# Kernel tuning notes

Hardware: AMD Instinct MI355X
Metric: run time of the kernel (lower is better)

## Reference

```python
import jax, jax.numpy as jnp
import numpy as np

VOL = 100.0  # cubic volume (100,100,100)


def _forward(x, positions, input_weights, features, output_weights,
             connection_radii, thresholds, n_iterations):
    # clamp positions into the volume (per-axis, min 0.1, max VOL-0.1)
    pos = jnp.clip(positions, 0.1, VOL - 0.1)                      # [N,3]
    radii = jnp.clip(connection_radii, 1.0, 50.0)                  # [N]
    # pairwise Euclidean distances via ||a||^2 + ||b||^2 - 2ab (avoids [N,N,3])
    sq = jnp.sum(pos * pos, axis=1)
    d2 = jnp.maximum(sq[:, None] + sq[None, :] - 2.0 * (pos @ pos.T), 0.0)
    pos_mask = d2 > 0.0
    dist = jnp.where(pos_mask, jnp.sqrt(jnp.where(pos_mask, d2, 1.0)), 0.0)  # [N,N]
    max_r = jnp.max(radii)
    conn_mask = (dist < max_r).astype(dist.dtype)
    atten = jnp.exp(-jnp.minimum(dist / (radii[:, None] + 1e-6), 20.0)) * conn_mask
    # feature similarity (F.normalize uses eps as a clamp-min on the norm)
    fn = features / jnp.maximum(jnp.linalg.norm(features, axis=1, keepdims=True), 1e-6)
    feat_sim = fn @ fn.T                                            # [N,N]
    cw = atten * (0.3 + 0.7 * jnp.clip(feat_sim, -1.0, 1.0))
    cw = cw / (jnp.sum(cw, axis=1, keepdims=True) + 1e-6)           # row-normalized [N,N]
    # spatial input / output gating along x-axis
    xc = jnp.clip(pos[:, 0] / VOL, 0.0, 1.0)                        # [N]
    iw = jnp.exp(-3.0 * xc)
    iw = iw / (jnp.sum(iw) + 1e-6)
    act = (x @ input_weights.T) * iw                                # [B,N]
    for _ in range(n_iterations):
        act = jnp.minimum(jax.nn.relu(act + act @ cw.T - thresholds), 100.0)
    ow = jnp.exp(3.0 * (xc - 1.0))
    ow = ow / (jnp.sum(ow) + 1e-6)
    return (act * ow) @ output_weights                              # [B,out]


def setup_inputs() -> dict:
    key = jax.random.key(0)
    ks = jax.random.split(key, 5)
    N, IN, OUT, FD, B = 8000, 784, 10, 32, 64
    return {
        "x": jax.random.normal(ks[0], (B, IN), jnp.float32),
        "positions": jax.random.uniform(ks[1], (N, 3), jnp.float32) * VOL,
        "input_weights": jax.random.normal(ks[2], (N, IN), jnp.float32) * 0.01,
        "features": jax.random.normal(ks[3], (N, FD), jnp.float32) * 0.1,
        "output_weights": jax.random.normal(ks[4], (N, OUT), jnp.float32) * 0.01,
        "connection_radii": jnp.ones((N,), jnp.float32) * 15.0,
        "thresholds": jnp.zeros((N,), jnp.float32),
        "n_iterations": 2,
    }


def reference(x, positions, input_weights, features, output_weights,
              connection_radii, thresholds, n_iterations):
    return _forward(x, positions, input_weights, features, output_weights,
                    connection_radii, thresholds, n_iterations)
```

## Files before the change

kernel.cpp:

```cpp
#include <hip/hip_runtime.h>
#include <hip/hip_bf16.h>
#include <math.h>

#define VOLF 100.0f
#define FD 32
#define OUT_DIM 10
#define MAXN 320
#define MAX_LAUNCH_ITERS 4
#define OB 128
#define CHUNK 28
#define NCHUNK 7
#define LDP 68
#define PS 8
#define NCD 5
#define CELLW 20.0f
#define NCELL (NCD*NCD)

__global__ __launch_bounds__(256) void k_prext(
    const float* __restrict__ x, const float* __restrict__ positions,
    const float* __restrict__ radii_in, const float* __restrict__ features,
    float* __restrict__ xT, float* __restrict__ posx4,
    float* __restrict__ radii, float* __restrict__ e_iw, float* __restrict__ e_ow,
    float* __restrict__ fn, float* __restrict__ scal, int N, int IN, int nxt)
{
    __shared__ float tile[64][65];
    __shared__ float red[256];
    if ((int)blockIdx.x < nxt) {
        int w = threadIdx.x >> 6, lane = threadIdx.x & 63;
        int k0 = blockIdx.x * 64;
        #pragma unroll
        for (int r = 0; r < 16; r++) {
            int b = w * 16 + r;
            int k = k0 + lane;
            if (k < IN) tile[lane][b] = x[(size_t)b * IN + k];
        }
        __syncthreads();
        #pragma unroll
        for (int r = 0; r < 16; r++) {
            int kl = w * 16 + r;
            int k = k0 + kl;
            if (k < IN) xT[(size_t)k * 64 + lane] = tile[kl][lane];
        }
        return;
    }
    int i = (blockIdx.x - nxt) * 256 + threadIdx.x;
    float my_iw = 0.0f, my_ow = 0.0f, my_r = 0.0f;
    if (i < N) {
        float px = fminf(fmaxf(positions[3*i+0], 0.1f), VOLF - 0.1f);
        float py = fminf(fmaxf(positions[3*i+1], 0.1f), VOLF - 0.1f);
        float pz = fminf(fmaxf(positions[3*i+2], 0.1f), VOLF - 0.1f);
        float sq = px*px + py*py + pz*pz;
        posx4[4*i+0] = px; posx4[4*i+1] = py; posx4[4*i+2] = pz; posx4[4*i+3] = sq;
        float r = fminf(fmaxf(radii_in[i], 1.0f), 50.0f);
        radii[i] = r; my_r = r;
        float xc = fminf(fmaxf(px / VOLF, 0.0f), 1.0f);
        my_iw = expf(-3.0f * xc);
        my_ow = expf(3.0f * (xc - 1.0f));
        e_iw[i] = my_iw; e_ow[i] = my_ow;
        float s = 0.0f;
        #pragma unroll
        for (int k = 0; k < FD; k++) { float v = features[(size_t)i*FD + k]; s += v*v; }
        float nrm = fmaxf(sqrtf(s), 1e-6f);
        #pragma unroll
        for (int k = 0; k < FD; k++) fn[(size_t)i*FD + k] = features[(size_t)i*FD + k] / nrm;
    }
    red[threadIdx.x] = my_iw; __syncthreads();
    for (int s = 128; s > 0; s >>= 1) { if (threadIdx.x < s) red[threadIdx.x] += red[threadIdx.x + s]; __syncthreads(); }
    if (threadIdx.x == 0) atomicAdd(&scal[0], red[0]);
    __syncthreads();
    red[threadIdx.x] = my_ow; __syncthreads();
    for (int s = 128; s > 0; s >>= 1) { if (threadIdx.x < s) red[threadIdx.x] += red[threadIdx.x + s]; __syncthreads(); }
    if (threadIdx.x == 0) atomicAdd(&scal[1], red[0]);
    if (i < N) atomicMax((int*)&scal[2], __float_as_int(my_r));
}

__global__ __launch_bounds__(64) void k_binfill(
    const float* __restrict__ posx4, float4* __restrict__ posb, int* __restrict__ jmap,
    int* __restrict__ binoff, int* __restrict__ bincnt, int N)
{
    int c = blockIdx.x, lane = threadIdx.x;
    int offs = 0, mine = 0;
    for (int jb = 0; jb < N; jb += 64) {
        float4 q = ((const float4*)posx4)[jb + lane];
        int ix = min(NCD-1, (int)(q.x * (1.0f/CELLW)));
        int iy = min(NCD-1, (int)(q.y * (1.0f/CELLW)));
        int cj = ix * NCD + iy;
        offs += (int)__popcll(__ballot(cj < c));
        mine += (int)__popcll(__ballot(cj == c));
    }
    unsigned long long lmask = (1ull << lane) - 1ull;
    int w = 0;
    for (int jb = 0; jb < N; jb += 64) {
        int j = jb + lane;
        float4 q = ((const float4*)posx4)[j];
        int ix = min(NCD-1, (int)(q.x * (1.0f/CELLW)));
        int iy = min(NCD-1, (int)(q.y * (1.0f/CELLW)));
        bool hit = (ix * NCD + iy == c);
        unsigned long long m = __ballot(hit);
        if (hit) {
            int pos = offs + w + (int)__popcll(m & lmask);
            posb[pos] = q;
            jmap[pos] = j;
        }
        w += (int)__popcll(m);
    }
    if (lane == 0) { binoff[c] = offs; bincnt[c] = mine; }
}

__global__ __launch_bounds__(256) void k_act0(
    const float* __restrict__ xT, const float* __restrict__ Wi,
    float* __restrict__ partial, int N, int IN)
{
    __shared__ float smem[2 * 64 * 68];
    float* wtT = smem;
    int t = threadIdx.x;
    int wave = t >> 6, lane = t & 63;
    int nr = lane >> 2, br = lane & 3;
    int i0 = blockIdx.x * 64;
    int kbase = blockIdx.y * 196;
    float acc[4][16];
    #pragma unroll
    for (int a = 0; a < 4; a++)
        #pragma unroll
        for (int b = 0; b < 16; b++) acc[a][b] = 0.0f;

    for (int c = 0; c < NCHUNK; c++) {
        int k0 = kbase + c * CHUNK;
        __syncthreads();
        for (int fi = t; fi < 64 * (CHUNK/4); fi += 256) {
            int n = fi / (CHUNK/4), q = fi % (CHUNK/4);
            float4 w4 = *(const float4*)(Wi + (size_t)(i0 + n) * IN + k0 + q * 4);
            wtT[(q*4+0)*LDP + n] = w4.x;
            wtT[(q*4+1)*LDP + n] = w4.y;
            wtT[(q*4+2)*LDP + n] = w4.z;
            wtT[(q*4+3)*LDP + n] = w4.w;
        }
        __syncthreads();
        for (int q = ((wave + c) & 3); q < CHUNK/4; q += 4) {
            #pragma unroll
            for (int j = 0; j < 4; j++) {
                int kl = q*4 + j;
                float4 a4 = *(const float4*)(&wtT[kl * LDP + nr*4]);
                const float* xr = xT + (size_t)(k0 + kl) * 64 + br*16;
                float4 b0 = *(const float4*)(xr + 0);
                float4 b1 = *(const float4*)(xr + 4);
                float4 b2 = *(const float4*)(xr + 8);
                float4 b3 = *(const float4*)(xr + 12);
                #pragma unroll
                for (int a = 0; a < 4; a++) {
                    float av = (a==0) ? a4.x : (a==1) ? a4.y : (a==2) ? a4.z : a4.w;
                    acc[a][ 0] += av*b0.x; acc[a][ 1] += av*b0.y; acc[a][ 2] += av*b0.z; acc[a][ 3] += av*b0.w;
                    acc[a][ 4] += av*b1.x; acc[a][ 5] += av*b1.y; acc[a][ 6] += av*b1.z; acc[a][ 7] += av*b1.w;
                    acc[a][ 8] += av*b2.x; acc[a][ 9] += av*b2.y; acc[a][10] += av*b2.z; acc[a][11] += av*b2.w;
                    acc[a][12] += av*b3.x; acc[a][13] += av*b3.y; acc[a][14] += av*b3.z; acc[a][15] += av*b3.w;
                }
            }
        }
    }
    __syncthreads();
    float4* sm4 = (float4*)smem;
    int g = wave >> 1;
    if (wave & 1) {
        #pragma unroll
        for (int a = 0; a < 4; a++)
            #pragma unroll
            for (int b4 = 0; b4 < 4; b4++)
                sm4[(g*16 + a*4 + b4) * 64 + lane] =
                    make_float4(acc[a][b4*4+0], acc[a][b4*4+1], acc[a][b4*4+2], acc[a][b4*4+3]);
    }
    __syncthreads();
    if (!(wave & 1)) {
        int slot = blockIdx.y * 2 + g;
        size_t pbase = ((size_t)slot * N + i0 + nr*4) * 64 + br*16;
        #pragma unroll
        for (int a = 0; a < 4; a++)
            #pragma unroll
            for (int b4 = 0; b4 < 4; b4++) {
                float4 o = sm4[(g*16 + a*4 + b4) * 64 + lane];
                o.x += acc[a][b4*4+0]; o.y += acc[a][b4*4+1];
                o.z += acc[a][b4*4+2]; o.w += acc[a][b4*4+3];
                *(float4*)(partial + pbase + (size_t)a * 64 + b4*4) = o;
            }
    }
}

__global__ __launch_bounds__(256) void k_act0_red(
    const float* __restrict__ partial, const float* __restrict__ e_iw,
    const float* __restrict__ scal, float* __restrict__ actA, int N)
{
    int idx = blockIdx.x * 256 + threadIdx.x;
    int i = idx >> 6;
    size_t stride = (size_t)N * 64;
    float s = 0.0f;
    #pragma unroll
    for (int p = 0; p < PS; p++) s += partial[p * stride + idx];
    float inv = 1.0f / (scal[0] + 1e-6f);
    actA[idx] = s * (e_iw[i] * inv);
}

__device__ __forceinline__ void scan_body(
    const float4& p, const float4& q, int j, float maxr, bool act,
    unsigned long long lmask, int2* __restrict__ ep, size_t base, int& cnt)
{
    float d2 = fmaxf(p.w + q.w - 2.0f*(p.x*q.x + p.y*q.y + p.z*q.z), 0.0f);
    float dist = sqrtf(d2);
    bool hit = act && (dist < maxr);
    unsigned long long m = __ballot(hit);
    if (m) {
        if (hit) {
            int pos = cnt + (int)__popcll(m & lmask);
            if (pos < MAXN) ep[base + pos] = make_int2(j, __float_as_int(dist));
        }
        cnt += (int)__popcll(m);
    }
}

__global__ __launch_bounds__(256) void k_scan(
    const float4* __restrict__ posb, const int* __restrict__ jmap,
    const float* __restrict__ scal, int2* __restrict__ ep, int* __restrict__ nbr_cnt,
    const int* __restrict__ binoff, const int* __restrict__ bincnt, int N)
{
    int wave = threadIdx.x >> 6, lane = threadIdx.x & 63;
    int s0 = (blockIdx.x * 4 + wave) * 2;
    float4 p0 = posb[s0], p1 = posb[s0 + 1];
    int r0 = jmap[s0], r1 = jmap[s0 + 1];
    float maxr = __int_as_float(((const int*)scal)[2]);
    int R = (int)ceilf(maxr * (1.0f/CELLW));
    int cxa = min(NCD-1, (int)(p0.x * (1.0f/CELLW))), cya = min(NCD-1, (int)(p0.y * (1.0f/CELLW)));
    int cxb = min(NCD-1, (int)(p1.x * (1.0f/CELLW))), cyb = min(NCD-1, (int)(p1.y * (1.0f/CELLW)));
    int ix0 = max(0, min(cxa, cxb) - R), ix1 = min(NCD-1, max(cxa, cxb) + R);
    int iy0 = max(0, min(cya, cyb) - R), iy1 = min(NCD-1, max(cya, cyb) + R);
    unsigned long long lmask = (1ull << lane) - 1ull;
    int c0 = 0, c1 = 0;
    size_t base0 = (size_t)r0 * MAXN, base1 = (size_t)r1 * MAXN;
    for (int ix = ix0; ix <= ix1; ix++)
    for (int iy = iy0; iy <= iy1; iy++) {
        int c = ix * NCD + iy;
        int bs = binoff[c], cnt = bincnt[c];
        for (int sb = 0; sb < cnt; sb += 64) {
            bool act = (sb + lane) < cnt;
            int s = act ? (bs + sb + lane) : bs;
            float4 q = posb[s];
            int j = jmap[s];
            scan_body(p0, q, j, maxr, act, lmask, ep, base0, c0);
            scan_body(p1, q, j, maxr, act, lmask, ep, base1, c1);
        }
    }
    if (lane == 0) {
        nbr_cnt[r0] = min(c0, MAXN);
        nbr_cnt[r1] = min(c1, MAXN);
    }
}

__global__ __launch_bounds__(256) void k_weight(
    const float* __restrict__ fn, const float* __restrict__ radii,
    int2* __restrict__ ep ,
    const int* __restrict__ nbr_cnt, float* __restrict__ rowinv, int N)
{
    int i = blockIdx.x;
    int lane = threadIdx.x & 63;
    int wave = threadIdx.x >> 6;
    int sub = lane & 7;
    int eg  = lane >> 3;
    float4 fni = ((const float4*)(fn + (size_t)i * FD))[sub];
    float inv_ri = 1.0f / (radii[i] + 1e-6f);
    int cnt = nbr_cnt[i];
    float s = 0.0f;
    for (int e0 = wave * 8; e0 < cnt; e0 += 32) {
        int e = e0 + eg;
        bool act = e < cnt;
        int ecl = act ? e : (cnt - 1);
        int2 edge = ep[(size_t)i * MAXN + ecl];
        int j      = edge.x;
        float dist = __int_as_float(edge.y);
        float4 fj = ((const float4*)(fn + (size_t)j * FD))[sub];
        float fs = fni.x*fj.x + fni.y*fj.y + fni.z*fj.z + fni.w*fj.w;
        fs += __shfl_xor(fs, 1, 64);
        fs += __shfl_xor(fs, 2, 64);
        fs += __shfl_xor(fs, 4, 64);
        fs = fminf(fmaxf(fs, -1.0f), 1.0f);
        float w = expf(-fminf(dist * inv_ri, 20.0f)) * (0.3f + 0.7f * fs);
        if (act && sub == 0) {
            ((float*)&ep[(size_t)i * MAXN + e])[1] = w;
            s += w;
        }
    }
    __shared__ float red[256];
    red[threadIdx.x] = s; __syncthreads();
    for (int st = 128; st > 0; st >>= 1) { if (threadIdx.x < st) red[threadIdx.x] += red[threadIdx.x + st]; __syncthreads(); }
    if (threadIdx.x == 0) rowinv[i] = 1.0f / (red[0] + 1e-6f);
}

__global__ __launch_bounds__(256) void k_iter(
    const float* __restrict__ actIn, float* __restrict__ actOut,
    const int2* __restrict__ ep, const int* __restrict__ nbr_cnt,
    const float* __restrict__ rowinv, const float* __restrict__ thr,
    const int* __restrict__ nIterPtr, int iterIdx, int N)
{
    if (iterIdx >= min(*nIterPtr, MAX_LAUNCH_ITERS)) return;
    int i = blockIdx.x;
    int wave = threadIdx.x >> 6, lane = threadIdx.x & 63;
    int cnt = nbr_cnt[i];
    float acc = 0.0f;
    for (int e = wave; e < cnt; e += 4) {
        int2 edge = ep[(size_t)i * MAXN + e];
        acc += actIn[(size_t)edge.x * 64 + lane] * __int_as_float(edge.y);
    }
    __shared__ float redA[4 * 64];
    redA[wave * 64 + lane] = acc;
    __syncthreads();
    if (wave == 0) {
        float tot = redA[lane] + redA[64 + lane] + redA[128 + lane] + redA[192 + lane];
        float v = actIn[(size_t)i * 64 + lane] + tot * rowinv[i] - thr[i];
        v = fminf(fmaxf(v, 0.0f), 100.0f);
        actOut[(size_t)i * 64 + lane] = v;
    }
}

__global__ __launch_bounds__(256) void k_out1(
    const float* __restrict__ actA, const float* __restrict__ actB,
    const int* __restrict__ nIterPtr, const float* __restrict__ e_ow,
    const float* __restrict__ scal, const float* __restrict__ outW,
    float* __restrict__ outPart, int N)
{
    int m = min(*nIterPtr, MAX_LAUNCH_ITERS);
    const float* actF = (m & 1) ? actB : actA;
    int wave = threadIdx.x >> 6, lane = threadIdx.x & 63;
    float inv = 1.0f / (scal[1] + 1e-6f);
    float acc[OUT_DIM];
    #pragma unroll
    for (int o = 0; o < OUT_DIM; o++) acc[o] = 0.0f;
    for (int i = blockIdx.x * 4 + wave; i < N; i += OB * 4) {
        float a = actF[(size_t)i * 64 + lane] * (e_ow[i] * inv);
        const float* wo = outW + (size_t)i * OUT_DIM;
        #pragma unroll
        for (int o = 0; o < OUT_DIM; o++) acc[o] += a * wo[o];
    }
    __shared__ float red[4][OUT_DIM][64];
    #pragma unroll
    for (int o = 0; o < OUT_DIM; o++) red[wave][o][lane] = acc[o];
    __syncthreads();
    if (wave == 0) {
        #pragma unroll
        for (int o = 0; o < OUT_DIM; o++) {
            float s = red[0][o][lane] + red[1][o][lane] + red[2][o][lane] + red[3][o][lane];
            outPart[((size_t)blockIdx.x * OUT_DIM + o) * 64 + lane] = s;
        }
    }
}

__global__ __launch_bounds__(256) void k_out2(
    const float* __restrict__ outPart, float* __restrict__ out)
{
    int t = blockIdx.x * 256 + threadIdx.x;
    if (t >= 64 * OUT_DIM) return;
    int b = t / OUT_DIM, o = t % OUT_DIM;
    float s = 0.0f;
    for (int blk = 0; blk < OB; blk++)
        s += outPart[((size_t)blk * OUT_DIM + o) * 64 + b];
    out[t] = s;
}

extern "C" void kernel_launch(void* const* d_in, const int* in_sizes, int n_in,
                              void* d_out, int out_size, void* d_ws, size_t ws_size,
                              hipStream_t stream)
{
    const float* x        = (const float*)d_in[0];
    const float* positions= (const float*)d_in[1];
    const float* Win      = (const float*)d_in[2];
    const float* features = (const float*)d_in[3];
    const float* Wout     = (const float*)d_in[4];
    const float* radii_in = (const float*)d_in[5];
    const float* thr      = (const float*)d_in[6];
    const int*   nIter    = (const int*)  d_in[7];

    const int N  = in_sizes[5];
    const int IN = in_sizes[2] / N;
    const int B  = in_sizes[0] / IN;
    (void)B;

    float* ws = (float*)d_ws;
    size_t off = 0;
    auto alloc = [&](size_t nfloats) { size_t cur = off; off += (nfloats + 63) & ~(size_t)63; return cur; };
    float* xT      = ws + alloc((size_t)B * IN);
    float* posx4   = ws + alloc((size_t)N * 4);
    float* radii   = ws + alloc(N);
    float* e_iw    = ws + alloc(N);
    float* e_ow    = ws + alloc(N);
    float* rowinv  = ws + alloc(N);
    float* scal    = ws + alloc(4);
    float* outPart = ws + alloc((size_t)OB * OUT_DIM * 64);
    float* fn      = ws + alloc((size_t)N * FD);
    float* actA    = ws + alloc((size_t)N * 64);
    float* actB    = ws + alloc((size_t)N * 64);
    float4* posb   = (float4*)(ws + alloc((size_t)N * 4));
    int*   jmap    = (int*)(ws + alloc(N));
    int*   binoff  = (int*)(ws + alloc(64));
    int*   bincnt  = (int*)(ws + alloc(64));
    int2*  ep      = (int2*)(ws + alloc((size_t)N * MAXN * 2));
    int*   nbr_cnt = (int*)(ws + alloc(N));
    float* partial = (float*)ep;

    hipMemsetAsync(scal, 0, 4 * sizeof(float), stream);

    int nxt = (IN + 63) / 64;
    int npre = (N + 255) / 256;
    k_prext<<<nxt + npre, 256, 0, stream>>>(x, positions, radii_in, features,
                                            xT, posx4, radii, e_iw, e_ow, fn, scal,
                                            N, IN, nxt);
    k_binfill<<<NCELL, 64, 0, stream>>>(posx4, posb, jmap, binoff, bincnt, N);
    k_act0<<<dim3(N / 64, 4), 256, 0, stream>>>(xT, Win, partial, N, IN);
    k_act0_red<<<(N * 64) / 256, 256, 0, stream>>>(partial, e_iw, scal, actA, N);
    k_scan<<<N / 8, 256, 0, stream>>>(posb, jmap, scal, ep, nbr_cnt, binoff, bincnt, N);
    k_weight<<<N, 256, 0, stream>>>(fn, radii, ep, nbr_cnt, rowinv, N);

    float* bufs[2] = {actA, actB};
    for (int it = 0; it < MAX_LAUNCH_ITERS; it++) {
        k_iter<<<N, 256, 0, stream>>>(bufs[it & 1], bufs[(it + 1) & 1],
                                      ep, nbr_cnt, rowinv, thr, nIter, it, N);
    }
    k_out1<<<OB, 256, 0, stream>>>(actA, actB, nIter, e_ow, scal, Wout, outPart, N);
    k_out2<<<3, 256, 0, stream>>>(outPart, (float*)d_out);
}
```

Before: 311.0 us.

## Replace serial per-cell binning with histogram, prefix scan and parallel scatter

The old binning kernel ran one 64-thread block per cell, and each block scanned all N points twice, so there were only 25 blocks and each did serial work over every point. Per-wavefront cell histograms are now built inside the preprocessing kernel, then a single-block prefix kernel computes per-group start offsets, and a 125-block scatter kernel places each point with a ballot rank. The order of points within each cell stays the same as before. In exchange it adds one extra kernel launch and a small serial prefix over 125 groups per cell.

New measurement: 259.8 us. 16.5% less time.

```diff
diff --git a/kernel.cpp b/kernel.cpp
--- a/kernel.cpp
+++ b/kernel.cpp
@@ -15,13 +15,16 @@
 #define NCD 5
 #define CELLW 20.0f
 #define NCELL (NCD*NCD)
+#define NG 125
+#define GP 128
 
 __global__ __launch_bounds__(256) void k_prext(
     const float* __restrict__ x, const float* __restrict__ positions,
     const float* __restrict__ radii_in, const float* __restrict__ features,
     float* __restrict__ xT, float* __restrict__ posx4,
     float* __restrict__ radii, float* __restrict__ e_iw, float* __restrict__ e_ow,
-    float* __restrict__ fn, float* __restrict__ scal, int N, int IN, int nxt)
+    float* __restrict__ fn, float* __restrict__ scal, int* __restrict__ hist,
+    int N, int IN, int nxt)
 {
     __shared__ float tile[64][65];
     __shared__ float red[256];
@@ -44,13 +47,18 @@
         return;
     }
     int i = (blockIdx.x - nxt) * 256 + threadIdx.x;
+    int lane = threadIdx.x & 63;
     float my_iw = 0.0f, my_ow = 0.0f, my_r = 0.0f;
+    int ci = 31;
     if (i < N) {
         float px = fminf(fmaxf(positions[3*i+0], 0.1f), VOLF - 0.1f);
         float py = fminf(fmaxf(positions[3*i+1], 0.1f), VOLF - 0.1f);
         float pz = fminf(fmaxf(positions[3*i+2], 0.1f), VOLF - 0.1f);
         float sq = px*px + py*py + pz*pz;
         posx4[4*i+0] = px; posx4[4*i+1] = py; posx4[4*i+2] = pz; posx4[4*i+3] = sq;
+        int ix = min(NCD-1, (int)(px * (1.0f/CELLW)));
+        int iy = min(NCD-1, (int)(py * (1.0f/CELLW)));
+        ci = ix * NCD + iy;
         float r = fminf(fmaxf(radii_in[i], 1.0f), 50.0f);
         radii[i] = r; my_r = r;
         float xc = fminf(fmaxf(px / VOLF, 0.0f), 1.0f);
@@ -64,6 +72,16 @@
         #pragma unroll
         for (int k = 0; k < FD; k++) fn[(size_t)i*FD + k] = features[(size_t)i*FD + k] / nrm;
     }
+    int g = i >> 6;
+    if (g < NG) {
+        int cnt = 0;
+        #pragma unroll
+        for (int c = 0; c < NCELL; c++) {
+            unsigned long long m = __ballot(ci == c);
+            if (lane == c) cnt = (int)__popcll(m);
+        }
+        if (lane < NCELL) hist[lane * GP + g] = cnt;
+    }
     red[threadIdx.x] = my_iw; __syncthreads();
     for (int s = 128; s > 0; s >>= 1) { if (threadIdx.x < s) red[threadIdx.x] += red[threadIdx.x + s]; __syncthreads(); }
     if (threadIdx.x == 0) atomicAdd(&scal[0], red[0]);
@@ -74,37 +92,54 @@
     if (i < N) atomicMax((int*)&scal[2], __float_as_int(my_r));
 }
 
-__global__ __launch_bounds__(64) void k_binfill(
-    const float* __restrict__ posx4, float4* __restrict__ posb, int* __restrict__ jmap,
-    int* __restrict__ binoff, int* __restrict__ bincnt, int N)
-{
-    int c = blockIdx.x, lane = threadIdx.x;
-    int offs = 0, mine = 0;
-    for (int jb = 0; jb < N; jb += 64) {
-        float4 q = ((const float4*)posx4)[jb + lane];
-        int ix = min(NCD-1, (int)(q.x * (1.0f/CELLW)));
-        int iy = min(NCD-1, (int)(q.y * (1.0f/CELLW)));
-        int cj = ix * NCD + iy;
-        offs += (int)__popcll(__ballot(cj < c));
-        mine += (int)__popcll(__ballot(cj == c));
-    }
+__global__ __launch_bounds__(64) void k_prefix(
+    const int* __restrict__ hist, int* __restrict__ start,
+    int* __restrict__ binoff, int* __restrict__ bincnt)
+{
+    __shared__ int tot[NCELL], boff[NCELL];
+    int lane = threadIdx.x;
+    if (lane < NCELL) {
+        int s = 0;
+        for (int g = 0; g < NG; g++) s += hist[lane * GP + g];
+        tot[lane] = s;
+    }
+    __syncthreads();
+    if (lane == 0) {
+        int s = 0;
+        for (int c = 0; c < NCELL; c++) { boff[c] = s; s += tot[c]; }
+    }
+    __syncthreads();
+    if (lane < NCELL) {
+        int s = boff[lane];
+        binoff[lane] = s;
+        bincnt[lane] = tot[lane];
+        for (int g = 0; g < NG; g++) {
+            start[lane * GP + g] = s;
+            s += hist[lane * GP + g];
+        }
+    }
+}
+
+__global__ __launch_bounds__(64) void k_scatter(
+    const float* __restrict__ posx4, const int* __restrict__ start,
+    float4* __restrict__ posb, int* __restrict__ jmap, int N)
+{
+    int g = blockIdx.x, lane = threadIdx.x;
+    int j = g * 64 + lane;
+    float4 q = ((const float4*)posx4)[j];
+    int ix = min(NCD-1, (int)(q.x * (1.0f/CELLW)));
+    int iy = min(NCD-1, (int)(q.y * (1.0f/CELLW)));
+    int ci = ix * NCD + iy;
     unsigned long long lmask = (1ull << lane) - 1ull;
-    int w = 0;
-    for (int jb = 0; jb < N; jb += 64) {
-        int j = jb + lane;
-        float4 q = ((const float4*)posx4)[j];
-        int ix = min(NCD-1, (int)(q.x * (1.0f/CELLW)));
-        int iy = min(NCD-1, (int)(q.y * (1.0f/CELLW)));
-        bool hit = (ix * NCD + iy == c);
-        unsigned long long m = __ballot(hit);
-        if (hit) {
-            int pos = offs + w + (int)__popcll(m & lmask);
-            posb[pos] = q;
-            jmap[pos] = j;
-        }
-        w += (int)__popcll(m);
-    }
-    if (lane == 0) { binoff[c] = offs; bincnt[c] = mine; }
+    int rank = 0;
+    #pragma unroll
+    for (int c = 0; c < NCELL; c++) {
+        unsigned long long m = __ballot(ci == c);
+        if (ci == c) rank = (int)__popcll(m & lmask);
+    }
+    int pos = start[ci * GP + g] + rank;
+    posb[pos] = q;
+    jmap[pos] = j;
 }
 
 __global__ __launch_bounds__(256) void k_act0(
@@ -395,6 +430,8 @@
     float* actB    = ws + alloc((size_t)N * 64);
     float4* posb   = (float4*)(ws + alloc((size_t)N * 4));
     int*   jmap    = (int*)(ws + alloc(N));
+    int*   hist    = (int*)(ws + alloc(NCELL * GP));
+    int*   startA  = (int*)(ws + alloc(NCELL * GP));
     int*   binoff  = (int*)(ws + alloc(64));
     int*   bincnt  = (int*)(ws + alloc(64));
     int2*  ep      = (int2*)(ws + alloc((size_t)N * MAXN * 2));
@@ -406,9 +443,10 @@
     int nxt = (IN + 63) / 64;
     int npre = (N + 255) / 256;
     k_prext<<<nxt + npre, 256, 0, stream>>>(x, positions, radii_in, features,
-                                            xT, posx4, radii, e_iw, e_ow, fn, scal,
+                                            xT, posx4, radii, e_iw, e_ow, fn, scal, hist,
                                             N, IN, nxt);
-    k_binfill<<<NCELL, 64, 0, stream>>>(posx4, posb, jmap, binoff, bincnt, N);
+    k_prefix<<<1, 64, 0, stream>>>(hist, startA, binoff, bincnt);
+    k_scatter<<<NG, 64, 0, stream>>>(posx4, startA, posb, jmap, N);
     k_act0<<<dim3(N / 64, 4), 256, 0, stream>>>(xT, Win, partial, N, IN);
     k_act0_red<<<(N * 64) / 256, 256, 0, stream>>>(partial, e_iw, scal, actA, N);
     k_scan<<<N / 8, 256, 0, stream>>>(posb, jmap, scal, ep, nbr_cnt, binoff, bincnt, N);
```
